# Performance work log

Hardware: AMD Instinct MI355X
Metric: run time of the kernel (lower is better)

The kernel has to match this reference:

```python
import jax, jax.numpy as jnp
import numpy as np

IN_FEATURES = 4096
OUT_FEATURES = 4096
M_TOKENS = 8192
WEIGHT_SCALE = 0.1
OUT_SCALE = 0.1


def setup_inputs() -> dict:
    key = jax.random.key(0)
    k_x, k_w = jax.random.split(key)
    # int8-valued activations and weights in [-128, 128), stored as int32 carriers
    x_q = jax.random.randint(k_x, (M_TOKENS, IN_FEATURES), 0, 256, dtype=jnp.int32) - 128
    weight_q = jax.random.randint(k_w, (OUT_FEATURES, IN_FEATURES), 0, 256, dtype=jnp.int32) - 128
    scale_x = jnp.float32(0.05)
    return {"x_q": x_q, "weight_q": weight_q, "scale_x": scale_x}


def reference(x_q, weight_q, scale_x):
    acc = jnp.einsum("mk,nk->mn", x_q.astype(jnp.int32), weight_q.astype(jnp.int32))
    # fused epilogue: rescale, round-to-nearest, saturate to int8
    scale = scale_x * jnp.float32(WEIGHT_SCALE) / jnp.float32(OUT_SCALE)
    y = acc.astype(jnp.float32) * scale
    y_q = jnp.clip(jnp.round(y), -128.0, 127.0).astype(jnp.int8)
    return (y_q, jnp.float32(OUT_SCALE))
```

## Files before the change

kernel.cpp:

```cpp
#include <hip/hip_runtime.h>
#include <stdint.h>

typedef int v4i  __attribute__((ext_vector_type(4)));
typedef int v16i __attribute__((ext_vector_type(16)));

#define M_TOK 8192
#define N_OUT 4096
#define K_IN  4096

#define BM 256
#define BN 256
#define BK 64
#define NT (K_IN / BK)
#define RING_STRIDE 32768
#define LDS_BYTES (4 * RING_STRIDE)

#define SGB __builtin_amdgcn_sched_group_barrier
#define SG_MFMA 0x8
#define SG_VMEM 0x20
#define SG_DSRD 0x100

__device__ __forceinline__ int pack4(int4 a) {
    return (a.x & 255) | ((a.y & 255) << 8) | ((a.z & 255) << 16) | ((a.w & 255) << 24);
}

__global__ __launch_bounds__(256) void pack_both(
    const int4* __restrict__ x, const int4* __restrict__ w,
    int* __restrict__ dA, int* __restrict__ dB, int n4x, int n4w)
{
    int i = blockIdx.x * blockDim.x + threadIdx.x;
    if (i < n4x) {
        dA[i] = pack4(x[i]);
    } else {
        int j = i - n4x;
        if (j < n4w) dB[j] = pack4(w[j]);
    }
}

__global__ __launch_bounds__(512, 2) void gemm_i8_kernel(
    const char* __restrict__ A8,
    const char* __restrict__ B8,
    const float* __restrict__ scale_ptr,
    float* __restrict__ out)
{
    extern __shared__ char lds[];

    const int tid  = threadIdx.x;
    const int wave = tid >> 6;
    const int lane = tid & 63;

    int wg = (blockIdx.x & 7) * 64 + (blockIdx.x >> 3);
    const int bx = wg >> 5;
    const int by = wg & 31;
    const int bm = by * BM;
    const int bn = bx * BN;

    const int wr = wave >> 2;
    const int wc = wave & 3;
    const int wm = wr * 128;
    const int wn = wc * 64;

    v16i acc[4][2];
#pragma unroll
    for (int mi = 0; mi < 4; ++mi)
#pragma unroll
        for (int nj = 0; nj < 2; ++nj)
#pragma unroll
            for (int r = 0; r < 16; ++r)
                acc[mi][nj][r] = 0;

    const int srow = lane >> 2;

    const char* gA[2]; const char* gB[2];
    int ldsAoff[2], ldsBoff[2];
#pragma unroll
    for (int q = 0; q < 2; ++q) {
        const int r0  = wave * 32 + q * 16;
        const int f   = ((srow >> 1) & 3) ^ ((srow >> 3) & 1) ^ (q << 1);
        const int sgr = (lane & 3) ^ f;
        gA[q] = A8 + (size_t)(bm + r0 + srow) * K_IN + sgr * 16;
        gB[q] = B8 + (size_t)(bn + r0 + srow) * K_IN + sgr * 16;
        ldsAoff[q] = r0 * 64;
        ldsBoff[q] = 16384 + r0 * 64;
    }

#define ISSUE(tile, q) do {                                                  \
        char* _rb = lds + ((tile) & 3) * RING_STRIDE;                        \
        const int _src = ((tile) < NT) ? (tile) : (NT - 1);                  \
        const int _k0 = _src * BK;                                           \
        __builtin_amdgcn_global_load_lds(                                    \
            (const __attribute__((address_space(1))) void*)(gA[q] + _k0),    \
            (__attribute__((address_space(3))) void*)(_rb + ldsAoff[q]),     \
            16, 0, 0);                                                       \
        __builtin_amdgcn_global_load_lds(                                    \
            (const __attribute__((address_space(1))) void*)(gB[q] + _k0),    \
            (__attribute__((address_space(3))) void*)(_rb + ldsBoff[q]),     \
            16, 0, 0);                                                       \
    } while (0)

    const int fm  = lane & 31;
    const int fh  = lane >> 5;
    const int fsw = ((fm >> 1) & 3) ^ ((fm >> 3) & 3);
    const int g0  = ((0 + fh) ^ fsw) << 4;
    const int g1  = ((2 + fh) ^ fsw) << 4;
    const int abase = (wm + fm) * 64;
    const int bbase = 16384 + (wn + fm) * 64;

    ISSUE(0, 0); ISSUE(0, 1);
    ISSUE(1, 0); ISSUE(1, 1);
    ISSUE(2, 0); ISSUE(2, 1);
    asm volatile("s_waitcnt vmcnt(8)" ::: "memory");
    __builtin_amdgcn_s_barrier();

    v4i a0[4], b0[2], a1[4], b1[2];
#pragma unroll
    for (int mi = 0; mi < 4; ++mi)
        a0[mi] = *(const v4i*)(lds + abase + mi * 2048 + g0);
#pragma unroll
    for (int nj = 0; nj < 2; ++nj)
        b0[nj] = *(const v4i*)(lds + bbase + nj * 2048 + g0);

    for (int t = 0; t < NT; ++t) {
        char* rb = lds + (t & 3) * RING_STRIDE;
        char* rn = lds + ((t + 1) & 3) * RING_STRIDE;

#pragma unroll
        for (int mi = 0; mi < 4; ++mi)
            a1[mi] = *(const v4i*)(rb + abase + mi * 2048 + g1);
#pragma unroll
        for (int nj = 0; nj < 2; ++nj)
            b1[nj] = *(const v4i*)(rb + bbase + nj * 2048 + g1);
        ISSUE(t + 3, 0);
#pragma unroll
        for (int mi = 0; mi < 4; ++mi)
#pragma unroll
            for (int nj = 0; nj < 2; ++nj)
                acc[mi][nj] = __builtin_amdgcn_mfma_i32_32x32x32_i8(
                    a0[mi], b0[nj], acc[mi][nj], 0, 0, 0);
        SGB(SG_DSRD, 1, 0); SGB(SG_MFMA, 1, 0);
        SGB(SG_DSRD, 1, 0); SGB(SG_MFMA, 1, 0);
        SGB(SG_DSRD, 1, 0); SGB(SG_MFMA, 1, 0);
        SGB(SG_DSRD, 1, 0); SGB(SG_MFMA, 1, 0);
        SGB(SG_DSRD, 1, 0); SGB(SG_MFMA, 1, 0);
        SGB(SG_DSRD, 1, 0); SGB(SG_MFMA, 1, 0);
        SGB(SG_VMEM, 1, 0); SGB(SG_MFMA, 1, 0);
        SGB(SG_VMEM, 1, 0); SGB(SG_MFMA, 1, 0);

        ISSUE(t + 3, 1);
        asm volatile("s_waitcnt vmcnt(8)" ::: "memory");
        __builtin_amdgcn_s_barrier();

#pragma unroll
        for (int mi = 0; mi < 4; ++mi)
            a0[mi] = *(const v4i*)(rn + abase + mi * 2048 + g0);
#pragma unroll
        for (int nj = 0; nj < 2; ++nj)
            b0[nj] = *(const v4i*)(rn + bbase + nj * 2048 + g0);
#pragma unroll
        for (int mi = 0; mi < 4; ++mi)
#pragma unroll
            for (int nj = 0; nj < 2; ++nj)
                acc[mi][nj] = __builtin_amdgcn_mfma_i32_32x32x32_i8(
                    a1[mi], b1[nj], acc[mi][nj], 0, 0, 0);
        SGB(SG_DSRD, 1, 0); SGB(SG_MFMA, 1, 0);
        SGB(SG_DSRD, 1, 0); SGB(SG_MFMA, 1, 0);
        SGB(SG_DSRD, 1, 0); SGB(SG_MFMA, 1, 0);
        SGB(SG_DSRD, 1, 0); SGB(SG_MFMA, 1, 0);
        SGB(SG_DSRD, 1, 0); SGB(SG_MFMA, 1, 0);
        SGB(SG_DSRD, 1, 0); SGB(SG_MFMA, 1, 0);
        SGB(SG_MFMA, 2, 0);
    }
#undef ISSUE

    const float s     = scale_ptr[0];
    const float scale = (s * 0.1f) / 0.1f;

#pragma unroll
    for (int mi = 0; mi < 4; ++mi) {
#pragma unroll
        for (int nj = 0; nj < 2; ++nj) {
#pragma unroll
            for (int r = 0; r < 16; ++r) {
                int row = bm + wm + mi * 32 + (r & 3) + 8 * (r >> 2) + 4 * fh;
                int col = bn + wn + nj * 32 + fm;
                float y = (float)acc[mi][nj][r] * scale;
                y = rintf(y);
                y = fminf(fmaxf(y, -128.0f), 127.0f);
                out[(size_t)row * N_OUT + col] = y;
            }
        }
    }

    if (bm == 0 && bn == 0 && tid == 0)
        out[(size_t)M_TOK * N_OUT] = 0.1f;
}

extern "C" void kernel_launch(void* const* d_in, const int* in_sizes, int n_in,
                              void* d_out, int out_size, void* d_ws, size_t ws_size,
                              hipStream_t stream)
{
    const int*   x_q     = (const int*)d_in[0];
    const int*   w_q     = (const int*)d_in[1];
    const float* scale_x = (const float*)d_in[2];
    float* out = (float*)d_out;

    char* A8 = (char*)d_ws;
    char* B8 = (char*)d_ws + (size_t)M_TOK * K_IN;

    const int n4x = (M_TOK * K_IN) / 4;
    const int n4w = (N_OUT * K_IN) / 4;

    static bool once = []{
        hipFuncSetAttribute(reinterpret_cast<const void*>(gemm_i8_kernel),
                            hipFuncAttributeMaxDynamicSharedMemorySize,
                            LDS_BYTES);
        return true;
    }();
    (void)once;

    pack_both<<<(n4x + n4w) / 256, 256, 0, stream>>>(
        (const int4*)x_q, (const int4*)w_q, (int*)A8, (int*)B8, n4x, n4w);

    gemm_i8_kernel<<<512, 512, LDS_BYTES, stream>>>(A8, B8, scale_x, out);
}
```

Before: 391.8 us.

## Pre-swizzle B into MFMA fragment layout and load it directly from global

The weight pack kernel now writes B in a per-32-row, per-32-K MFMA fragment order, so each lane can read its B operand with one 16-byte global load. B no longer goes through LDS. The LDS ring shrinks to A only, and the schedule barriers are rebalanced to interleave the new global B loads with MFMAs. This trades LDS traffic and footprint for direct global/L2 reads of B with little latency hiding, since B is fetched only about one half-tile ahead and B reuse across waves now relies on cache.

```diff
diff --git a/kernel.cpp b/kernel.cpp
--- a/kernel.cpp
+++ b/kernel.cpp
@@ -7,33 +7,43 @@
 #define M_TOK 8192
 #define N_OUT 4096
 #define K_IN  4096
+#define KT_N  (K_IN / 32)
 
 #define BM 256
 #define BN 256
 #define BK 64
 #define NT (K_IN / BK)
-#define RING_STRIDE 32768
-#define LDS_BYTES (4 * RING_STRIDE)
+#define SLOT_A 16384
+#define LDS_BYTES (4 * SLOT_A)
 
 #define SGB __builtin_amdgcn_sched_group_barrier
 #define SG_MFMA 0x8
 #define SG_VMEM 0x20
 #define SG_DSRD 0x100
 
+
 __device__ __forceinline__ int pack4(int4 a) {
     return (a.x & 255) | ((a.y & 255) << 8) | ((a.z & 255) << 16) | ((a.w & 255) << 24);
 }
 
 __global__ __launch_bounds__(256) void pack_both(
     const int4* __restrict__ x, const int4* __restrict__ w,
-    int* __restrict__ dA, int* __restrict__ dB, int n4x, int n4w)
+    int* __restrict__ dA, int* __restrict__ dB, int n4x, int ntB)
 {
     int i = blockIdx.x * blockDim.x + threadIdx.x;
     if (i < n4x) {
         dA[i] = pack4(x[i]);
     } else {
         int j = i - n4x;
-        if (j < n4w) dB[j] = pack4(w[j]);
+        if (j >= ntB) return;
+        const int r  = j >> 8;
+        const int k0 = (j & 255) << 4;
+        const int4* p = w + ((size_t)r * K_IN + k0) / 4;
+        int4 c0 = p[0], c1 = p[1], c2 = p[2], c3 = p[3];
+        const int kt   = k0 >> 5;
+        const int lane = (r & 31) + (((k0 >> 4) & 1) << 5);
+        int* q = dB + ((((size_t)(r >> 5) * KT_N + kt) << 8) + (lane << 2));
+        q[0] = pack4(c0); q[1] = pack4(c1); q[2] = pack4(c2); q[3] = pack4(c3);
     }
 }
 
@@ -71,30 +81,22 @@
 
     const int srow = lane >> 2;
 
-    const char* gA[2]; const char* gB[2];
-    int ldsAoff[2], ldsBoff[2];
+    const char* gA[2]; int ldsAoff[2];
 #pragma unroll
     for (int q = 0; q < 2; ++q) {
         const int r0  = wave * 32 + q * 16;
         const int f   = ((srow >> 1) & 3) ^ ((srow >> 3) & 1) ^ (q << 1);
         const int sgr = (lane & 3) ^ f;
         gA[q] = A8 + (size_t)(bm + r0 + srow) * K_IN + sgr * 16;
-        gB[q] = B8 + (size_t)(bn + r0 + srow) * K_IN + sgr * 16;
         ldsAoff[q] = r0 * 64;
-        ldsBoff[q] = 16384 + r0 * 64;
-    }
-
-#define ISSUE(tile, q) do {                                                  \
-        char* _rb = lds + ((tile) & 3) * RING_STRIDE;                        \
+    }
+
+#define ISSUE_A(tile, q) do {                                                \
+        char* _rb = lds + ((tile) & 3) * SLOT_A;                             \
         const int _src = ((tile) < NT) ? (tile) : (NT - 1);                  \
-        const int _k0 = _src * BK;                                           \
         __builtin_amdgcn_global_load_lds(                                    \
-            (const __attribute__((address_space(1))) void*)(gA[q] + _k0),    \
+            (const __attribute__((address_space(1))) void*)(gA[q] + _src * BK), \
             (__attribute__((address_space(3))) void*)(_rb + ldsAoff[q]),     \
-            16, 0, 0);                                                       \
-        __builtin_amdgcn_global_load_lds(                                    \
-            (const __attribute__((address_space(1))) void*)(gB[q] + _k0),    \
-            (__attribute__((address_space(3))) void*)(_rb + ldsBoff[q]),     \
             16, 0, 0);                                                       \
     } while (0)
 
@@ -104,12 +106,16 @@
     const int g0  = ((0 + fh) ^ fsw) << 4;
     const int g1  = ((2 + fh) ^ fsw) << 4;
     const int abase = (wm + fm) * 64;
-    const int bbase = 16384 + (wn + fm) * 64;
-
-    ISSUE(0, 0); ISSUE(0, 1);
-    ISSUE(1, 0); ISSUE(1, 1);
-    ISSUE(2, 0); ISSUE(2, 1);
-    asm volatile("s_waitcnt vmcnt(8)" ::: "memory");
+
+    const char* pB[2];
+#pragma unroll
+    for (int nj = 0; nj < 2; ++nj)
+        pB[nj] = B8 + (((size_t)((bn + wn) / 32 + nj) * KT_N) << 10) + lane * 16;
+
+    ISSUE_A(0, 0); ISSUE_A(0, 1);
+    ISSUE_A(1, 0); ISSUE_A(1, 1);
+    ISSUE_A(2, 0); ISSUE_A(2, 1);
+    asm volatile("s_waitcnt vmcnt(4)" ::: "memory");
     __builtin_amdgcn_s_barrier();
 
     v4i a0[4], b0[2], a1[4], b1[2];
@@ -118,19 +124,21 @@
         a0[mi] = *(const v4i*)(lds + abase + mi * 2048 + g0);
 #pragma unroll
     for (int nj = 0; nj < 2; ++nj)
-        b0[nj] = *(const v4i*)(lds + bbase + nj * 2048 + g0);
+        b0[nj] = *(const v4i*)(pB[nj] + 0);
 
     for (int t = 0; t < NT; ++t) {
-        char* rb = lds + (t & 3) * RING_STRIDE;
-        char* rn = lds + ((t + 1) & 3) * RING_STRIDE;
+        char* rb = lds + (t & 3) * SLOT_A;
+        char* rn = lds + ((t + 1) & 3) * SLOT_A;
+        const int ktB1 = 2 * t + 1;
+        const int ktB0 = (2 * t + 2 < 2 * NT) ? 2 * t + 2 : 2 * NT - 2;
 
 #pragma unroll
         for (int mi = 0; mi < 4; ++mi)
             a1[mi] = *(const v4i*)(rb + abase + mi * 2048 + g1);
 #pragma unroll
         for (int nj = 0; nj < 2; ++nj)
-            b1[nj] = *(const v4i*)(rb + bbase + nj * 2048 + g1);
-        ISSUE(t + 3, 0);
+            b1[nj] = *(const v4i*)(pB[nj] + (ktB1 << 10));
+        ISSUE_A(t + 3, 0);
 #pragma unroll
         for (int mi = 0; mi < 4; ++mi)
 #pragma unroll
@@ -141,12 +149,11 @@
         SGB(SG_DSRD, 1, 0); SGB(SG_MFMA, 1, 0);
         SGB(SG_DSRD, 1, 0); SGB(SG_MFMA, 1, 0);
         SGB(SG_DSRD, 1, 0); SGB(SG_MFMA, 1, 0);
-        SGB(SG_DSRD, 1, 0); SGB(SG_MFMA, 1, 0);
-        SGB(SG_DSRD, 1, 0); SGB(SG_MFMA, 1, 0);
         SGB(SG_VMEM, 1, 0); SGB(SG_MFMA, 1, 0);
         SGB(SG_VMEM, 1, 0); SGB(SG_MFMA, 1, 0);
-
-        ISSUE(t + 3, 1);
+        SGB(SG_VMEM, 1, 0); SGB(SG_MFMA, 2, 0);
+
+        ISSUE_A(t + 3, 1);
         asm volatile("s_waitcnt vmcnt(8)" ::: "memory");
         __builtin_amdgcn_s_barrier();
 
@@ -155,7 +162,7 @@
             a0[mi] = *(const v4i*)(rn + abase + mi * 2048 + g0);
 #pragma unroll
         for (int nj = 0; nj < 2; ++nj)
-            b0[nj] = *(const v4i*)(rn + bbase + nj * 2048 + g0);
+            b0[nj] = *(const v4i*)(pB[nj] + (ktB0 << 10));
 #pragma unroll
         for (int mi = 0; mi < 4; ++mi)
 #pragma unroll
@@ -166,11 +173,10 @@
         SGB(SG_DSRD, 1, 0); SGB(SG_MFMA, 1, 0);
         SGB(SG_DSRD, 1, 0); SGB(SG_MFMA, 1, 0);
         SGB(SG_DSRD, 1, 0); SGB(SG_MFMA, 1, 0);
-        SGB(SG_DSRD, 1, 0); SGB(SG_MFMA, 1, 0);
-        SGB(SG_DSRD, 1, 0); SGB(SG_MFMA, 1, 0);
-        SGB(SG_MFMA, 2, 0);
-    }
-#undef ISSUE
+        SGB(SG_VMEM, 1, 0); SGB(SG_MFMA, 1, 0);
+        SGB(SG_VMEM, 1, 0); SGB(SG_MFMA, 3, 0);
+    }
+#undef ISSUE_A
 
     const float s     = scale_ptr[0];
     const float scale = (s * 0.1f) / 0.1f;
@@ -208,7 +214,7 @@
     char* B8 = (char*)d_ws + (size_t)M_TOK * K_IN;
 
     const int n4x = (M_TOK * K_IN) / 4;
-    const int n4w = (N_OUT * K_IN) / 4;
+    const int ntB = N_OUT * (K_IN / 16);
 
     static bool once = []{
         hipFuncSetAttribute(reinterpret_cast<const void*>(gemm_i8_kernel),
@@ -218,8 +224,8 @@
     }();
     (void)once;
 
-    pack_both<<<(n4x + n4w) / 256, 256, 0, stream>>>(
-        (const int4*)x_q, (const int4*)w_q, (int*)A8, (int*)B8, n4x, n4w);
+    pack_both<<<(n4x + ntB) / 256, 256, 0, stream>>>(
+        (const int4*)x_q, (const int4*)w_q, (int*)A8, (int*)B8, n4x, ntB);
 
     gemm_i8_kernel<<<512, 512, LDS_BYTES, stream>>>(A8, B8, scale_x, out);
 }
```

Measured after the change: 452.9 us. +15.6%, slower.

## Use 4 waves per block with 128x128 per-wave tiles

Applied to the files above, without the earlier changes.

Halves the workgroup from 8 to 4 waves, so each wave now computes a 128x128 output tile (4x4 MFMA accumulators) instead of 128x64, and issues 4 global-to-LDS loads per operand per tile. The schedule-group barriers and vmcnt thresholds are adjusted to the larger MFMA count. This raises per-wave register reuse and MFMA density and reduces LDS reads per MFMA, at the cost of much higher register pressure (256 accumulator registers), lower occupancy and fewer waves to hide latency.

```diff
diff --git a/kernel.cpp b/kernel.cpp
--- a/kernel.cpp
+++ b/kernel.cpp
@@ -37,7 +37,7 @@
     }
 }
 
-__global__ __launch_bounds__(512, 2) void gemm_i8_kernel(
+__global__ __launch_bounds__(256, 1) void gemm_i8_kernel(
     const char* __restrict__ A8,
     const char* __restrict__ B8,
     const float* __restrict__ scale_ptr,
@@ -55,47 +55,52 @@
     const int bm = by * BM;
     const int bn = bx * BN;
 
-    const int wr = wave >> 2;
-    const int wc = wave & 3;
-    const int wm = wr * 128;
-    const int wn = wc * 64;
-
-    v16i acc[4][2];
+    const int wm = (wave >> 1) * 128;
+    const int wn = (wave & 1) * 128;
+
+    v16i acc[4][4];
 #pragma unroll
     for (int mi = 0; mi < 4; ++mi)
 #pragma unroll
-        for (int nj = 0; nj < 2; ++nj)
+        for (int nj = 0; nj < 4; ++nj)
 #pragma unroll
             for (int r = 0; r < 16; ++r)
                 acc[mi][nj][r] = 0;
 
-    const int srow = lane >> 2;
-
-    const char* gA[2]; const char* gB[2];
-    int ldsAoff[2], ldsBoff[2];
-#pragma unroll
-    for (int q = 0; q < 2; ++q) {
-        const int r0  = wave * 32 + q * 16;
-        const int f   = ((srow >> 1) & 3) ^ ((srow >> 3) & 1) ^ (q << 1);
-        const int sgr = (lane & 3) ^ f;
+    const int srow  = lane >> 2;
+    const int fbase = ((srow >> 1) & 3) ^ ((srow >> 3) & 1);
+
+    const char* gA[4]; const char* gB[4];
+    int ldsAoff[4], ldsBoff[4];
+#pragma unroll
+    for (int q = 0; q < 4; ++q) {
+        const int r0  = wave * 64 + q * 16;
+        const int sgr = (lane & 3) ^ fbase ^ ((q & 1) << 1);
         gA[q] = A8 + (size_t)(bm + r0 + srow) * K_IN + sgr * 16;
         gB[q] = B8 + (size_t)(bn + r0 + srow) * K_IN + sgr * 16;
         ldsAoff[q] = r0 * 64;
         ldsBoff[q] = 16384 + r0 * 64;
     }
 
-#define ISSUE(tile, q) do {                                                  \
+#define ISSUE_A(tile) do {                                                   \
         char* _rb = lds + ((tile) & 3) * RING_STRIDE;                        \
-        const int _src = ((tile) < NT) ? (tile) : (NT - 1);                  \
-        const int _k0 = _src * BK;                                           \
-        __builtin_amdgcn_global_load_lds(                                    \
-            (const __attribute__((address_space(1))) void*)(gA[q] + _k0),    \
-            (__attribute__((address_space(3))) void*)(_rb + ldsAoff[q]),     \
-            16, 0, 0);                                                       \
-        __builtin_amdgcn_global_load_lds(                                    \
-            (const __attribute__((address_space(1))) void*)(gB[q] + _k0),    \
-            (__attribute__((address_space(3))) void*)(_rb + ldsBoff[q]),     \
-            16, 0, 0);                                                       \
+        const int _k0 = (((tile) < NT) ? (tile) : (NT - 1)) * BK;            \
+        _Pragma("unroll")                                                    \
+        for (int _q = 0; _q < 4; ++_q)                                       \
+            __builtin_amdgcn_global_load_lds(                                \
+                (const __attribute__((address_space(1))) void*)(gA[_q]+_k0), \
+                (__attribute__((address_space(3))) void*)(_rb+ldsAoff[_q]),  \
+                16, 0, 0);                                                   \
+    } while (0)
+#define ISSUE_B(tile) do {                                                   \
+        char* _rb = lds + ((tile) & 3) * RING_STRIDE;                        \
+        const int _k0 = (((tile) < NT) ? (tile) : (NT - 1)) * BK;            \
+        _Pragma("unroll")                                                    \
+        for (int _q = 0; _q < 4; ++_q)                                       \
+            __builtin_amdgcn_global_load_lds(                                \
+                (const __attribute__((address_space(1))) void*)(gB[_q]+_k0), \
+                (__attribute__((address_space(3))) void*)(_rb+ldsBoff[_q]),  \
+                16, 0, 0);                                                   \
     } while (0)
 
     const int fm  = lane & 31;
@@ -106,18 +111,18 @@
     const int abase = (wm + fm) * 64;
     const int bbase = 16384 + (wn + fm) * 64;
 
-    ISSUE(0, 0); ISSUE(0, 1);
-    ISSUE(1, 0); ISSUE(1, 1);
-    ISSUE(2, 0); ISSUE(2, 1);
-    asm volatile("s_waitcnt vmcnt(8)" ::: "memory");
+    ISSUE_A(0); ISSUE_B(0);
+    ISSUE_A(1); ISSUE_B(1);
+    ISSUE_A(2); ISSUE_B(2);
+    asm volatile("s_waitcnt vmcnt(16)" ::: "memory");
     __builtin_amdgcn_s_barrier();
 
-    v4i a0[4], b0[2], a1[4], b1[2];
+    v4i a0[4], b0[4], a1[4], b1[4];
 #pragma unroll
     for (int mi = 0; mi < 4; ++mi)
         a0[mi] = *(const v4i*)(lds + abase + mi * 2048 + g0);
 #pragma unroll
-    for (int nj = 0; nj < 2; ++nj)
+    for (int nj = 0; nj < 4; ++nj)
         b0[nj] = *(const v4i*)(lds + bbase + nj * 2048 + g0);
 
     for (int t = 0; t < NT; ++t) {
@@ -128,13 +133,13 @@
         for (int mi = 0; mi < 4; ++mi)
             a1[mi] = *(const v4i*)(rb + abase + mi * 2048 + g1);
 #pragma unroll
-        for (int nj = 0; nj < 2; ++nj)
+        for (int nj = 0; nj < 4; ++nj)
             b1[nj] = *(const v4i*)(rb + bbase + nj * 2048 + g1);
-        ISSUE(t + 3, 0);
-#pragma unroll
-        for (int mi = 0; mi < 4; ++mi)
-#pragma unroll
-            for (int nj = 0; nj < 2; ++nj)
+        ISSUE_A(t + 3);
+#pragma unroll
+        for (int mi = 0; mi < 4; ++mi)
+#pragma unroll
+            for (int nj = 0; nj < 4; ++nj)
                 acc[mi][nj] = __builtin_amdgcn_mfma_i32_32x32x32_i8(
                     a0[mi], b0[nj], acc[mi][nj], 0, 0, 0);
         SGB(SG_DSRD, 1, 0); SGB(SG_MFMA, 1, 0);
@@ -143,23 +148,27 @@
         SGB(SG_DSRD, 1, 0); SGB(SG_MFMA, 1, 0);
         SGB(SG_DSRD, 1, 0); SGB(SG_MFMA, 1, 0);
         SGB(SG_DSRD, 1, 0); SGB(SG_MFMA, 1, 0);
+        SGB(SG_DSRD, 1, 0); SGB(SG_MFMA, 1, 0);
+        SGB(SG_DSRD, 1, 0); SGB(SG_MFMA, 1, 0);
         SGB(SG_VMEM, 1, 0); SGB(SG_MFMA, 1, 0);
         SGB(SG_VMEM, 1, 0); SGB(SG_MFMA, 1, 0);
-
-        ISSUE(t + 3, 1);
-        asm volatile("s_waitcnt vmcnt(8)" ::: "memory");
+        SGB(SG_VMEM, 1, 0); SGB(SG_MFMA, 1, 0);
+        SGB(SG_VMEM, 1, 0); SGB(SG_MFMA, 4, 0);
+
+        ISSUE_B(t + 3);
+        asm volatile("s_waitcnt vmcnt(16)" ::: "memory");
         __builtin_amdgcn_s_barrier();
 
 #pragma unroll
         for (int mi = 0; mi < 4; ++mi)
             a0[mi] = *(const v4i*)(rn + abase + mi * 2048 + g0);
 #pragma unroll
-        for (int nj = 0; nj < 2; ++nj)
+        for (int nj = 0; nj < 4; ++nj)
             b0[nj] = *(const v4i*)(rn + bbase + nj * 2048 + g0);
 #pragma unroll
         for (int mi = 0; mi < 4; ++mi)
 #pragma unroll
-            for (int nj = 0; nj < 2; ++nj)
+            for (int nj = 0; nj < 4; ++nj)
                 acc[mi][nj] = __builtin_amdgcn_mfma_i32_32x32x32_i8(
                     a1[mi], b1[nj], acc[mi][nj], 0, 0, 0);
         SGB(SG_DSRD, 1, 0); SGB(SG_MFMA, 1, 0);
@@ -168,9 +177,11 @@
         SGB(SG_DSRD, 1, 0); SGB(SG_MFMA, 1, 0);
         SGB(SG_DSRD, 1, 0); SGB(SG_MFMA, 1, 0);
         SGB(SG_DSRD, 1, 0); SGB(SG_MFMA, 1, 0);
-        SGB(SG_MFMA, 2, 0);
-    }
-#undef ISSUE
+        SGB(SG_DSRD, 1, 0); SGB(SG_MFMA, 1, 0);
+        SGB(SG_DSRD, 1, 0); SGB(SG_MFMA, 8, 0);
+    }
+#undef ISSUE_A
+#undef ISSUE_B
 
     const float s     = scale_ptr[0];
     const float scale = (s * 0.1f) / 0.1f;
@@ -178,7 +189,7 @@
 #pragma unroll
     for (int mi = 0; mi < 4; ++mi) {
 #pragma unroll
-        for (int nj = 0; nj < 2; ++nj) {
+        for (int nj = 0; nj < 4; ++nj) {
 #pragma unroll
             for (int r = 0; r < 16; ++r) {
                 int row = bm + wm + mi * 32 + (r & 3) + 8 * (r >> 2) + 4 * fh;
@@ -221,5 +232,5 @@
     pack_both<<<(n4x + n4w) / 256, 256, 0, stream>>>(
         (const int4*)x_q, (const int4*)w_q, (int*)A8, (int*)B8, n4x, n4w);
 
-    gemm_i8_kernel<<<512, 512, LDS_BYTES, stream>>>(A8, B8, scale_x, out);
-}
+    gemm_i8_kernel<<<512, 256, LDS_BYTES, stream>>>(A8, B8, scale_x, out);
+}
```

Measured after the change: 708.4 us. 80.8% more time.
